# Kernel tuning notes

Hardware: AMD Instinct MI355X
Metric: run time of the kernel (lower is better)

Reference implementation:

```python
import jax, jax.numpy as jnp
import numpy as np

B, L = 2, 1024
V, D_MODEL, NL = 32, 256, 6
DI, DS, DC, DTR = 512, 16, 4, 16  # d_inner=expand*d_model, d_state, d_conv, dt_rank=d_model/16
NC, MAXL = 10, 2048
ALPHA = 0.1  # observer_alpha


def setup_inputs() -> dict:
    key = jax.random.key(0)
    ks = jax.random.split(key, 16)
    std = 0.02
    emb = std * jax.random.normal(ks[0], (V, D_MODEL), jnp.float32)
    emb = emb.at[0].set(0.0)  # padding_idx=0
    pos_emb = std * jax.random.normal(ks[1], (MAXL, D_MODEL), jnp.float32)
    ln_w = jnp.ones((NL, D_MODEL), jnp.float32)
    ln_b = jnp.zeros((NL, D_MODEL), jnp.float32)
    in_proj_w = std * jax.random.normal(ks[2], (NL, 2 * DI, D_MODEL), jnp.float32)
    conv_w = 0.1 * jax.random.normal(ks[3], (NL, DI, DC), jnp.float32)
    conv_b = jnp.zeros((NL, DI), jnp.float32)
    x_proj_w = std * jax.random.normal(ks[4], (NL, DTR + 2 * DS, DI), jnp.float32)
    dt_proj_w = std * jax.random.normal(ks[5], (NL, DI, DTR), jnp.float32)
    dt_proj_b = jnp.full((NL, DI), -4.6, jnp.float32)  # softplus(-4.6) ~ 0.01 init dt
    A_log = jnp.broadcast_to(jnp.log(jnp.arange(1, DS + 1, dtype=jnp.float32)), (NL, DI, DS)).copy()  # S4D-real
    Dp = jnp.ones((NL, DI), jnp.float32)
    out_proj_w = std * jax.random.normal(ks[6], (NL, D_MODEL, DI), jnp.float32)
    norm_w = jnp.ones((D_MODEL,), jnp.float32)
    norm_b = jnp.zeros((D_MODEL,), jnp.float32)
    cls_w = std * jax.random.normal(ks[7], (NC, D_MODEL), jnp.float32)
    cls_b = jnp.zeros((NC,), jnp.float32)
    x = jax.random.randint(ks[8], (B, L), 0, V, jnp.int64 if jax.config.jax_enable_x64 else jnp.int32)
    mask = jnp.ones((B, L), jnp.int32)
    return dict(emb=emb, pos_emb=pos_emb, ln_w=ln_w, ln_b=ln_b, in_proj_w=in_proj_w,
                conv_w=conv_w, conv_b=conv_b, x_proj_w=x_proj_w, dt_proj_w=dt_proj_w,
                dt_proj_b=dt_proj_b, A_log=A_log, Dp=Dp, out_proj_w=out_proj_w,
                norm_w=norm_w, norm_b=norm_b, cls_w=cls_w, cls_b=cls_b, x=x, mask=mask)


def _ln(x, w, b):
    m = x.mean(-1, keepdims=True)
    v = ((x - m) ** 2).mean(-1, keepdims=True)
    return (x - m) / jnp.sqrt(v + 1e-5) * w + b


def _forward(emb, pos_emb, ln_w, ln_b, in_proj_w, conv_w, conv_b, x_proj_w,
             dt_proj_w, dt_proj_b, A_log, Dp, out_proj_w, norm_w, norm_b,
             cls_w, cls_b, x, mask):
    Bsz, Lsz = x.shape
    h = emb[x] + pos_emb[:Lsz][None, :, :]  # [B,L,D]
    for i in range(NL):
        res = h
        hn = _ln(h, ln_w[i], ln_b[i])
        xz = hn @ in_proj_w[i].T                      # [B,L,2*DI]
        x_in, z = jnp.split(xz, 2, axis=-1)
        # causal depthwise conv1d, kernel DC
        xpad = jnp.pad(x_in, ((0, 0), (DC - 1, 0), (0, 0)))
        xc = conv_b[i]
        for k in range(DC):
            xc = xc + conv_w[i][:, k] * xpad[:, k:k + Lsz, :]
        xc = jax.nn.silu(xc)
        x_dbl = xc @ x_proj_w[i].T                    # [B,L,DTR+2*DS]
        dt = x_dbl[..., :DTR]
        Bm = x_dbl[..., DTR:DTR + DS]
        Cm = x_dbl[..., DTR + DS:]
        delta = jax.nn.softplus(dt @ dt_proj_w[i].T + dt_proj_b[i])  # [B,L,DI]
        A = -jnp.exp(A_log[i])                        # [DI,DS]
        dA = jnp.exp(delta[..., None] * A)            # [B,L,DI,DS]
        dBu = delta[..., None] * Bm[:, :, None, :] * xc[..., None]

        def step(carry, inp):
            hs, hh = carry
            dA_t, dBu_t, c_t = inp
            hs = dA_t * hs + dBu_t                    # true state
            pred = dA_t * hh + dBu_t                  # observer prediction
            hh = pred + ALPHA * (hs - pred)           # Luenberger correction
            y = jnp.einsum('bdn,bn->bd', hh, c_t)
            return (hs, hh), y

        init = (jnp.zeros((Bsz, DI, DS), xc.dtype), jnp.zeros((Bsz, DI, DS), xc.dtype))
        _, ys = jax.lax.scan(step, init,
                             (jnp.moveaxis(dA, 1, 0), jnp.moveaxis(dBu, 1, 0), jnp.moveaxis(Cm, 1, 0)))
        y = jnp.moveaxis(ys, 0, 1) + Dp[i] * xc       # [B,L,DI]
        y = y * jax.nn.silu(z)
        h = y @ out_proj_w[i].T + res
    mf = mask[..., None].astype(h.dtype)
    pooled = (h * mf).sum(axis=1) / mf.sum(axis=1)    # masked mean pool
    pooled = _ln(pooled, norm_w, norm_b)
    return pooled @ cls_w.T + cls_b                   # [B,NC]


def reference(emb, pos_emb, ln_w, ln_b, in_proj_w, conv_w, conv_b, x_proj_w,
              dt_proj_w, dt_proj_b, A_log, Dp, out_proj_w, norm_w, norm_b,
              cls_w, cls_b, x, mask):
    return _forward(emb, pos_emb, ln_w, ln_b, in_proj_w, conv_w, conv_b, x_proj_w,
                    dt_proj_w, dt_proj_b, A_log, Dp, out_proj_w, norm_w, norm_b,
                    cls_w, cls_b, x, mask)
```

## Files before the change

### kernel.cpp

```cpp
#include <hip/hip_runtime.h>
#include <math.h>

#define B_ 2
#define L_ 1024
#define DM 256
#define NL_ 6
#define DI_ 512
#define DS_ 16
#define DC_ 4
#define NC_ 10
#define ALPHA_ 0.1f
#define LC 32
#define NCH (L_/LC)
#define NCHAIN (B_*DI_*DS_)
#define BETA_LC 0.034336838202925124f

typedef unsigned short ushort_t;
typedef __attribute__((ext_vector_type(8))) short s16x8;
typedef __attribute__((ext_vector_type(4))) float f32x4;
typedef __attribute__((ext_vector_type(8))) unsigned short u16x8;

__device__ __forceinline__ float sigmoidf_(float x){ return 1.f/(1.f+__expf(-x)); }
__device__ __forceinline__ ushort_t f2bf(float f){
  union{float f;unsigned u;} c; c.f=f; unsigned u=c.u;
  return (ushort_t)((u + 0x7fffu + ((u>>16)&1u))>>16);
}
__device__ __forceinline__ float bf2f(ushort_t h){
  union{unsigned u;float f;} c; c.u = ((unsigned)h)<<16; return c.f;
}

__global__ void k_embed(const float* __restrict__ emb, const float* __restrict__ pos,
                        const int* __restrict__ ids, float* __restrict__ h){
  int row = blockIdx.x;
  int t = row & (L_-1);
  int d = threadIdx.x;
  int v = ids[row];
  h[(size_t)row*DM + d] = emb[(size_t)v*DM + d] + pos[(size_t)t*DM + d];
}

__global__ void k_cvt(const float* __restrict__ in, ushort_t* __restrict__ o, int n){
  int i = (blockIdx.x*256 + threadIdx.x)*4;
  if (i < n){
    float4 v = *reinterpret_cast<const float4*>(&in[i]);
    ushort4 r;
    r.x = f2bf(v.x); r.y = f2bf(v.y); r.z = f2bf(v.z); r.w = f2bf(v.w);
    *reinterpret_cast<ushort4*>(&o[i]) = r;
  }
}

__global__ __launch_bounds__(256) void k_gemm_ln(const float* __restrict__ h,
    const ushort_t* __restrict__ W, const float* __restrict__ lw,
    const float* __restrict__ lb, ushort_t* __restrict__ xzb){
  __shared__ ushort_t As[64][264];
  __shared__ ushort_t Ws[64][264];
  int bm = blockIdx.y<<6, bn = blockIdx.x<<6;
  int tid = threadIdx.x;
  {
    int r = tid>>2, q = tid&3;
    const float* src = &h[(size_t)(bm+r)*DM + q*64];
    float4 v[16]; float s1=0.f, s2=0.f;
    #pragma unroll
    for (int i=0;i<16;i++){
      v[i] = *reinterpret_cast<const float4*>(src + i*4);
      s1 += v[i].x+v[i].y+v[i].z+v[i].w;
      s2 += v[i].x*v[i].x+v[i].y*v[i].y+v[i].z*v[i].z+v[i].w*v[i].w;
    }
    s1 += __shfl_xor(s1,1); s2 += __shfl_xor(s2,1);
    s1 += __shfl_xor(s1,2); s2 += __shfl_xor(s2,2);
    float mean = s1*(1.f/DM);
    float rstd = rsqrtf(s2*(1.f/DM) - mean*mean + 1e-5f);
    #pragma unroll
    for (int i=0;i<16;i++){
      int c = q*64 + i*4;
      ushort4 o;
      o.x = f2bf((v[i].x-mean)*rstd*lw[c+0]+lb[c+0]);
      o.y = f2bf((v[i].y-mean)*rstd*lw[c+1]+lb[c+1]);
      o.z = f2bf((v[i].z-mean)*rstd*lw[c+2]+lb[c+2]);
      o.w = f2bf((v[i].w-mean)*rstd*lw[c+3]+lb[c+3]);
      *reinterpret_cast<ushort4*>(&As[r][c]) = o;
    }
    const ushort_t* ws = &W[(size_t)(bn+r)*DM + q*64];
    #pragma unroll
    for (int i=0;i<8;i++)
      *reinterpret_cast<u16x8*>(&Ws[r][q*64+i*8]) = *reinterpret_cast<const u16x8*>(ws + i*8);
  }
  __syncthreads();
  int lane = tid&63, wid = tid>>6;
  int wm = (wid>>1)<<5, wn = (wid&1)<<5;
  int fr = lane&15, fk = (lane>>4)<<3;
  f32x4 acc[2][2] = {};
  #pragma unroll
  for (int k0=0;k0<DM;k0+=32){
    s16x8 a0 = *reinterpret_cast<const s16x8*>(&As[wm+fr][k0+fk]);
    s16x8 a1 = *reinterpret_cast<const s16x8*>(&As[wm+16+fr][k0+fk]);
    s16x8 b0 = *reinterpret_cast<const s16x8*>(&Ws[wn+fr][k0+fk]);
    s16x8 b1 = *reinterpret_cast<const s16x8*>(&Ws[wn+16+fr][k0+fk]);
    acc[0][0] = __builtin_amdgcn_mfma_f32_16x16x32_bf16(a0,b0,acc[0][0],0,0,0);
    acc[0][1] = __builtin_amdgcn_mfma_f32_16x16x32_bf16(a0,b1,acc[0][1],0,0,0);
    acc[1][0] = __builtin_amdgcn_mfma_f32_16x16x32_bf16(a1,b0,acc[1][0],0,0,0);
    acc[1][1] = __builtin_amdgcn_mfma_f32_16x16x32_bf16(a1,b1,acc[1][1],0,0,0);
  }
  int cr = (lane>>4)<<2, cc = lane&15;
  #pragma unroll
  for (int i=0;i<2;i++)
    #pragma unroll
    for (int j=0;j<2;j++){
      int row = bm + wm + (i<<4) + cr;
      int col = bn + wn + (j<<4) + cc;
      #pragma unroll
      for (int r=0;r<4;r++)
        xzb[(size_t)(row+r)*(2*DI_) + col] = f2bf(acc[i][j][r]);
    }
}

__global__ __launch_bounds__(256) void k_xpc(const ushort_t* __restrict__ xzb,
    const float* __restrict__ cw, const float* __restrict__ cb,
    const float* __restrict__ xw, const float* __restrict__ dtw,
    const float* __restrict__ dtb, float* __restrict__ xc,
    float* __restrict__ xdbl, float* __restrict__ delta){
  __shared__ float sxz[7][DI_];
  __shared__ float sx[4][DI_];
  __shared__ float sdbl[4][48];
  int tid = threadIdx.x;
  int m0 = blockIdx.x*4;
  #pragma unroll
  for (int idx=0; idx<14; ++idx){
    int flat = idx*256 + tid;
    int i = flat>>9, d = flat&511;
    int mr = m0 - 3 + i;
    sxz[i][d] = (mr>=0) ? bf2f(xzb[(size_t)mr*(2*DI_) + d]) : 0.f;
  }
  __syncthreads();
  #pragma unroll
  for (int idx=0; idx<8; ++idx){
    int flat = idx*256 + tid;
    int r = flat>>9, d = flat&511;
    int t = (m0 + r) & (L_-1);
    float acc = cb[d];
    #pragma unroll
    for (int k=0;k<4;k++)
      if (t-3+k >= 0) acc = fmaf(cw[d*4+k], sxz[r+k][d], acc);
    float sv = acc * sigmoidf_(acc);
    sx[r][d] = sv;
    xc[(size_t)(m0+r)*DI_ + d] = sv;
  }
  __syncthreads();
  if (tid < 192){
    int o = tid>>2, q = tid&3;
    const float* wp = &xw[(size_t)o*DI_ + q*128];
    float a0=0.f,a1=0.f,a2=0.f,a3=0.f;
    #pragma unroll 8
    for (int k4=0;k4<32;k4++){
      float4 wv = *reinterpret_cast<const float4*>(wp + k4*4);
      int kk = q*128 + k4*4;
      float4 x0 = *reinterpret_cast<const float4*>(&sx[0][kk]);
      float4 x1 = *reinterpret_cast<const float4*>(&sx[1][kk]);
      float4 x2 = *reinterpret_cast<const float4*>(&sx[2][kk]);
      float4 x3 = *reinterpret_cast<const float4*>(&sx[3][kk]);
      a0 = fmaf(x0.x,wv.x,a0); a0 = fmaf(x0.y,wv.y,a0); a0 = fmaf(x0.z,wv.z,a0); a0 = fmaf(x0.w,wv.w,a0);
      a1 = fmaf(x1.x,wv.x,a1); a1 = fmaf(x1.y,wv.y,a1); a1 = fmaf(x1.z,wv.z,a1); a1 = fmaf(x1.w,wv.w,a1);
      a2 = fmaf(x2.x,wv.x,a2); a2 = fmaf(x2.y,wv.y,a2); a2 = fmaf(x2.z,wv.z,a2); a2 = fmaf(x2.w,wv.w,a2);
      a3 = fmaf(x3.x,wv.x,a3); a3 = fmaf(x3.y,wv.y,a3); a3 = fmaf(x3.z,wv.z,a3); a3 = fmaf(x3.w,wv.w,a3);
    }
    a0 += __shfl_xor(a0,1); a0 += __shfl_xor(a0,2);
    a1 += __shfl_xor(a1,1); a1 += __shfl_xor(a1,2);
    a2 += __shfl_xor(a2,1); a2 += __shfl_xor(a2,2);
    a3 += __shfl_xor(a3,1); a3 += __shfl_xor(a3,2);
    if (q==0){
      sdbl[0][o]=a0; sdbl[1][o]=a1; sdbl[2][o]=a2; sdbl[3][o]=a3;
      xdbl[(size_t)(m0+0)*48+o]=a0;
      xdbl[(size_t)(m0+1)*48+o]=a1;
      xdbl[(size_t)(m0+2)*48+o]=a2;
      xdbl[(size_t)(m0+3)*48+o]=a3;
    }
  }
  __syncthreads();
  #pragma unroll
  for (int idx=0; idx<8; ++idx){
    int flat = idx*256 + tid;
    int r = flat>>9, n = flat&511;
    const float4* wp = reinterpret_cast<const float4*>(&dtw[n*16]);
    float4 w0=wp[0], w1=wp[1], w2=wp[2], w3=wp[3];
    const float* sd = sdbl[r];
    float acc = dtb[n];
    acc = fmaf(sd[0],w0.x,acc);  acc = fmaf(sd[1],w0.y,acc);
    acc = fmaf(sd[2],w0.z,acc);  acc = fmaf(sd[3],w0.w,acc);
    acc = fmaf(sd[4],w1.x,acc);  acc = fmaf(sd[5],w1.y,acc);
    acc = fmaf(sd[6],w1.z,acc);  acc = fmaf(sd[7],w1.w,acc);
    acc = fmaf(sd[8],w2.x,acc);  acc = fmaf(sd[9],w2.y,acc);
    acc = fmaf(sd[10],w2.z,acc); acc = fmaf(sd[11],w2.w,acc);
    acc = fmaf(sd[12],w3.x,acc); acc = fmaf(sd[13],w3.y,acc);
    acc = fmaf(sd[14],w3.z,acc); acc = fmaf(sd[15],w3.w,acc);
    delta[(size_t)(m0+r)*DI_ + n] = (acc>20.f)? acc : log1pf(__expf(acc));
  }
}

__global__ __launch_bounds__(256) void k_scanA(const float* __restrict__ delta,
    const float* __restrict__ xc, const float* __restrict__ xdbl,
    const float* __restrict__ A_log, float* __restrict__ cpArr,
    float* __restrict__ slocArr, float* __restrict__ hlocArr){
  int j = blockIdx.x, g = blockIdx.y, b = blockIdx.z;
  int tid = threadIdx.x;
  int n = tid&15, dg = tid>>4;
  int d0 = g*16;
  __shared__ float sdel[LC][16], sxv[LC][16], sB[LC][16];
  #pragma unroll
  for (int idx=0; idx<2; ++idx){
    int flat = idx*256 + tid;
    int t = flat>>4, c = flat&15;
    int m = b*L_ + j*LC + t;
    sdel[t][c] = delta[(size_t)m*DI_ + d0 + c];
    sxv[t][c]  = xc  [(size_t)m*DI_ + d0 + c];
    sB[t][c]   = xdbl[(size_t)m*48 + 16 + c];
  }
  __syncthreads();
  float a = -__expf(A_log[(d0+dg)*DS_ + n]);
  float dA[LC], dBu[LC];
  #pragma unroll
  for (int t=0;t<LC;t++){
    float dv = sdel[t][dg];
    dA[t]  = __expf(dv*a);
    dBu[t] = dv * sxv[t][dg] * sB[t][n];
  }
  float hs=0.f, hh=0.f, cp=1.f;
  #pragma unroll
  for (int t=0;t<LC;t++){
    float mix = fmaf(ALPHA_, hs-hh, hh);
    hs = fmaf(dA[t], hs, dBu[t]);
    hh = fmaf(dA[t], mix, dBu[t]);
    cp *= dA[t];
  }
  size_t o = (size_t)j*NCHAIN + (size_t)(b*DI_+d0)*DS_ + tid;
  cpArr[o]=cp; slocArr[o]=hs; hlocArr[o]=hh;
}

__global__ __launch_bounds__(256) void k_scanC(const float* __restrict__ delta,
    const float* __restrict__ xc, const float* __restrict__ xdbl,
    const ushort_t* __restrict__ xzb, const float* __restrict__ A_log,
    const float* __restrict__ Dp, const float* __restrict__ cpArr,
    const float* __restrict__ slocArr, const float* __restrict__ hlocArr,
    ushort_t* __restrict__ y2b){
  int j = blockIdx.x, g = blockIdx.y, b = blockIdx.z;
  int tid = threadIdx.x;
  int n = tid&15, dg = tid>>4;
  int d0 = g*16;
  __shared__ float sdel[LC][16], sxv[LC][16], sB[LC][16], sC[LC][16], sz[LC][16], sy[LC][16];
  #pragma unroll
  for (int idx=0; idx<2; ++idx){
    int flat = idx*256 + tid;
    int t = flat>>4, c = flat&15;
    int m = b*L_ + j*LC + t;
    sdel[t][c] = delta[(size_t)m*DI_ + d0 + c];
    sxv[t][c]  = xc  [(size_t)m*DI_ + d0 + c];
    sB[t][c]   = xdbl[(size_t)m*48 + 16 + c];
    sC[t][c]   = xdbl[(size_t)m*48 + 32 + c];
    sz[t][c]   = bf2f(xzb[(size_t)m*(2*DI_) + DI_ + d0 + c]);
  }
  int chain = (b*DI_+d0)*DS_ + tid;
  float hs=0.f, hh=0.f;
  #pragma unroll 4
  for (int jj=0; jj<j; ++jj){
    size_t o = (size_t)jj*NCHAIN + chain;
    float cp = cpArr[o], sl = slocArr[o], hl = hlocArr[o];
    float snew = fmaf(cp, hs, sl);
    hh = fmaf(cp, fmaf(BETA_LC, hh-hs, hs), hl);
    hs = snew;
  }
  __syncthreads();
  float a = -__expf(A_log[(d0+dg)*DS_ + n]);
  float dA[LC], dBu[LC];
  #pragma unroll
  for (int t=0;t<LC;t++){
    float dv = sdel[t][dg];
    dA[t]  = __expf(dv*a);
    dBu[t] = dv * sxv[t][dg] * sB[t][n];
  }
  float yv[LC];
  #pragma unroll
  for (int t=0;t<LC;t++){
    float mix = fmaf(ALPHA_, hs-hh, hh);
    hs = fmaf(dA[t], hs, dBu[t]);
    hh = fmaf(dA[t], mix, dBu[t]);
    yv[t] = hh * sC[t][n];
  }
  #pragma unroll
  for (int t=0;t<LC;t++){
    yv[t] += __shfl_xor(yv[t],1,16);
    yv[t] += __shfl_xor(yv[t],2,16);
    yv[t] += __shfl_xor(yv[t],4,16);
    yv[t] += __shfl_xor(yv[t],8,16);
  }
  if (n==0){
    #pragma unroll
    for (int t=0;t<LC;t++) sy[t][dg] = yv[t];
  }
  __syncthreads();
  float dpv = Dp[d0 + (tid&15)];
  #pragma unroll
  for (int idx=0; idx<2; ++idx){
    int flat = idx*256 + tid;
    int t2 = flat>>4, dd = flat&15;
    float xvv = sxv[t2][dd];
    float zv  = sz [t2][dd];
    float yfin = (sy[t2][dd] + dpv*xvv) * (zv*sigmoidf_(zv));
    y2b[(size_t)(b*L_ + j*LC + t2)*DI_ + d0 + dd] = f2bf(yfin);
  }
}

__global__ __launch_bounds__(256) void k_gemm_out(const ushort_t* __restrict__ A,
    const ushort_t* __restrict__ W, float* __restrict__ h){
  __shared__ ushort_t As[32][264];
  __shared__ ushort_t Ws[64][264];
  int bm = blockIdx.y<<5, bn = blockIdx.x<<6;
  int tid = threadIdx.x;
  int lane = tid&63, wid = tid>>6;
  int wm = (wid>>1)<<4, wn = (wid&1)<<5;
  int fr = lane&15, fk = (lane>>4)<<3;
  f32x4 acc[2] = {};
  for (int k0=0;k0<DI_;k0+=256){
    {
      int r = tid>>3, q = tid&7;
      const ushort_t* src = &A[(size_t)(bm+r)*DI_ + k0 + q*32];
      #pragma unroll
      for (int i=0;i<4;i++)
        *reinterpret_cast<u16x8*>(&As[r][q*32+i*8]) = *reinterpret_cast<const u16x8*>(src+i*8);
      int r2 = tid>>2, q2 = tid&3;
      const ushort_t* ws = &W[(size_t)(bn+r2)*DI_ + k0 + q2*64];
      #pragma unroll
      for (int i=0;i<8;i++)
        *reinterpret_cast<u16x8*>(&Ws[r2][q2*64+i*8]) = *reinterpret_cast<const u16x8*>(ws+i*8);
    }
    __syncthreads();
    #pragma unroll
    for (int k=0;k<256;k+=32){
      s16x8 a0 = *reinterpret_cast<const s16x8*>(&As[wm+fr][k+fk]);
      s16x8 b0 = *reinterpret_cast<const s16x8*>(&Ws[wn+fr][k+fk]);
      s16x8 b1 = *reinterpret_cast<const s16x8*>(&Ws[wn+16+fr][k+fk]);
      acc[0] = __builtin_amdgcn_mfma_f32_16x16x32_bf16(a0,b0,acc[0],0,0,0);
      acc[1] = __builtin_amdgcn_mfma_f32_16x16x32_bf16(a0,b1,acc[1],0,0,0);
    }
    __syncthreads();
  }
  int cr = (lane>>4)<<2, cc = lane&15;
  #pragma unroll
  for (int jj=0;jj<2;jj++){
    int row = bm + wm + cr;
    int col = bn + wn + (jj<<4) + cc;
    #pragma unroll
    for (int r=0;r<4;r++){
      size_t idx2 = (size_t)(row+r)*DM + col;
      h[idx2] += acc[jj][r];
    }
  }
}

__global__ __launch_bounds__(256) void k_pool(const float* __restrict__ h,
    const int* __restrict__ mask, float* __restrict__ partial){
  int p = blockIdx.x, b = blockIdx.y, d = threadIdx.x;
  int t0 = p*64;
  __shared__ float sm[64];
  if (d < 64) sm[d] = (float)mask[b*L_ + t0 + d];
  __syncthreads();
  const float* hp = &h[(size_t)(b*L_ + t0)*DM + d];
  float s = 0.f;
  #pragma unroll 8
  for (int i=0;i<64;i++)
    s = fmaf(sm[i], hp[(size_t)i*DM], s);
  partial[(size_t)(b*16+p)*DM + d] = s;
}

__global__ __launch_bounds__(256) void k_head(const float* __restrict__ partial,
    const int* __restrict__ mask, const float* __restrict__ nw, const float* __restrict__ nb,
    const float* __restrict__ cw, const float* __restrict__ cb, float* __restrict__ out){
  int b = blockIdx.x, d = threadIdx.x;
  int4 mi = *reinterpret_cast<const int4*>(&mask[b*L_ + d*4]);
  float cnt = (float)(mi.x + mi.y + mi.z + mi.w);
  #pragma unroll
  for (int o=32;o>0;o>>=1) cnt += __shfl_down(cnt,o);
  __shared__ float ac[4];
  __shared__ float scnt;
  int wid = d>>6, lane = d&63;
  if (lane==0) ac[wid] = cnt;
  __syncthreads();
  if (d==0) scnt = ac[0]+ac[1]+ac[2]+ac[3];
  __syncthreads();
  float s = 0.f;
  #pragma unroll
  for (int p=0;p<16;p++) s += partial[(size_t)(b*16+p)*DM + d];
  float v = s / scnt;
  float s1 = v, s2 = v*v;
  #pragma unroll
  for (int o=32;o>0;o>>=1){ s1 += __shfl_down(s1,o); s2 += __shfl_down(s2,o); }
  __shared__ float a1[4], a2[4];
  __shared__ float mv[2];
  if (lane==0){ a1[wid]=s1; a2[wid]=s2; }
  __syncthreads();
  if (d==0){
    float t1=a1[0]+a1[1]+a1[2]+a1[3];
    float t2=a2[0]+a2[1]+a2[2]+a2[3];
    float m = t1/(float)DM;
    mv[0]=m; mv[1]=rsqrtf(t2/(float)DM - m*m + 1e-5f);
  }
  __syncthreads();
  __shared__ float sp[DM];
  sp[d] = (v-mv[0])*mv[1]*nw[d]+nb[d];
  __syncthreads();
  __shared__ float cpart[NC_][16];
  if (d < NC_*16){
    int c = d>>4, q = d&15;
    float acc = 0.f;
    #pragma unroll
    for (int k=0;k<16;k++) acc = fmaf(sp[q*16+k], cw[(size_t)c*DM+q*16+k], acc);
    cpart[c][q] = acc;
  }
  __syncthreads();
  if (d < NC_){
    float acc = cb[d];
    #pragma unroll
    for (int q=0;q<16;q++) acc += cpart[d][q];
    out[b*NC_+d] = acc;
  }
}

extern "C" void kernel_launch(void* const* d_in, const int* in_sizes, int n_in,
                              void* d_out, int out_size, void* d_ws, size_t ws_size,
                              hipStream_t stream){
  const float* emb   = (const float*)d_in[0];
  const float* pos   = (const float*)d_in[1];
  const float* ln_w  = (const float*)d_in[2];
  const float* ln_b  = (const float*)d_in[3];
  const float* ipw   = (const float*)d_in[4];
  const float* cw    = (const float*)d_in[5];
  const float* cb    = (const float*)d_in[6];
  const float* xpw   = (const float*)d_in[7];
  const float* dtw   = (const float*)d_in[8];
  const float* dtb   = (const float*)d_in[9];
  const float* A_log = (const float*)d_in[10];
  const float* Dp    = (const float*)d_in[11];
  const float* opw   = (const float*)d_in[12];
  const float* nw    = (const float*)d_in[13];
  const float* nb    = (const float*)d_in[14];
  const float* clw   = (const float*)d_in[15];
  const float* clb   = (const float*)d_in[16];
  const int*   ids   = (const int*)d_in[17];
  const int*   mask  = (const int*)d_in[18];
  float* out = (float*)d_out;

  float* ws    = (float*)d_ws;
  float* h     = ws;
  float* xc    = h + 524288;
  float* xdbl  = xc + 1048576;
  float* delta = xdbl + 98304;
  float* cpA   = delta + 1048576;
  float* slocA = cpA + 524288;
  float* hlocA = slocA + 524288;
  float* part  = hlocA + 524288;
  ushort_t* xzb  = (ushort_t*)(part + 8192);
  ushort_t* y2b  = xzb + 2097152;
  ushort_t* ipwb = y2b + 1048576;
  ushort_t* opwb = ipwb + 1572864;

  k_cvt<<<dim3(1536), 256, 0, stream>>>(ipw, ipwb, 6*2*DI_*DM);
  k_cvt<<<dim3(768),  256, 0, stream>>>(opw, opwb, 6*DM*DI_);
  k_embed<<<dim3(B_*L_), dim3(DM), 0, stream>>>(emb, pos, ids, h);

  for (int l=0; l<NL_; ++l){
    k_gemm_ln<<<dim3(16, 32), 256, 0, stream>>>(
        h, ipwb + (size_t)l*2*DI_*DM, ln_w + l*DM, ln_b + l*DM, xzb);
    k_xpc<<<dim3((B_*L_)/4), 256, 0, stream>>>(
        xzb, cw + l*DI_*DC_, cb + l*DI_, xpw + (size_t)l*48*DI_,
        dtw + (size_t)l*DI_*16, dtb + l*DI_, xc, xdbl, delta);
    k_scanA<<<dim3(NCH, DI_/16, B_), 256, 0, stream>>>(
        delta, xc, xdbl, A_log + (size_t)l*DI_*DS_, cpA, slocA, hlocA);
    k_scanC<<<dim3(NCH, DI_/16, B_), 256, 0, stream>>>(
        delta, xc, xdbl, xzb, A_log + (size_t)l*DI_*DS_, Dp + l*DI_,
        cpA, slocA, hlocA, y2b);
    k_gemm_out<<<dim3(DM/64, (B_*L_)/32), 256, 0, stream>>>(
        y2b, opwb + (size_t)l*DM*DI_, h);
  }
  k_pool<<<dim3(16, B_), 256, 0, stream>>>(h, mask, part);
  k_head<<<dim3(B_), 256, 0, stream>>>(part, mask, nw, nb, clw, clb, out);
}
```

Baseline: 479.1 us.

## Store scan inputs in bf16, pack chunk summaries, vectorize loads, merge weight conversion

xc and delta are now stored as bf16 instead of fp32, and scanA/scanC load them with 16-byte vector reads. The per-chunk summaries (cp, hs, hh) are packed into one float4 array instead of three separate arrays. The scan loops run in 8-step slabs to lower register pressure, the x-proj shared array is padded to avoid bank conflicts, and the two weight-conversion launches are merged into one. The intent is to cut global memory traffic and launch overhead, at the cost of bf16 rounding of delta and xc before the scan, which adds numerical error.

```diff
diff --git a/kernel.cpp b/kernel.cpp
--- a/kernel.cpp
+++ b/kernel.cpp
@@ -28,6 +28,7 @@
 __device__ __forceinline__ float bf2f(ushort_t h){
   union{unsigned u;float f;} c; c.u = ((unsigned)h)<<16; return c.f;
 }
+__device__ __forceinline__ int kidx(int d){ return d + ((d>>7)<<2); }
 
 __global__ void k_embed(const float* __restrict__ emb, const float* __restrict__ pos,
                         const int* __restrict__ ids, float* __restrict__ h){
@@ -38,14 +39,17 @@
   h[(size_t)row*DM + d] = emb[(size_t)v*DM + d] + pos[(size_t)t*DM + d];
 }
 
-__global__ void k_cvt(const float* __restrict__ in, ushort_t* __restrict__ o, int n){
+__global__ void k_cvt2(const float* __restrict__ a, int na, const float* __restrict__ b2,
+                       ushort_t* __restrict__ oa, ushort_t* __restrict__ ob, int ntot){
   int i = (blockIdx.x*256 + threadIdx.x)*4;
-  if (i < n){
-    float4 v = *reinterpret_cast<const float4*>(&in[i]);
-    ushort4 r;
-    r.x = f2bf(v.x); r.y = f2bf(v.y); r.z = f2bf(v.z); r.w = f2bf(v.w);
-    *reinterpret_cast<ushort4*>(&o[i]) = r;
-  }
+  if (i >= ntot) return;
+  const float* src; ushort_t* dst; int k;
+  if (i < na){ src = a; dst = oa; k = i; }
+  else       { src = b2; dst = ob; k = i - na; }
+  float4 v = *reinterpret_cast<const float4*>(&src[k]);
+  ushort4 r;
+  r.x = f2bf(v.x); r.y = f2bf(v.y); r.z = f2bf(v.z); r.w = f2bf(v.w);
+  *reinterpret_cast<ushort4*>(&dst[k]) = r;
 }
 
 __global__ __launch_bounds__(256) void k_gemm_ln(const float* __restrict__ h,
@@ -116,10 +120,10 @@
 __global__ __launch_bounds__(256) void k_xpc(const ushort_t* __restrict__ xzb,
     const float* __restrict__ cw, const float* __restrict__ cb,
     const float* __restrict__ xw, const float* __restrict__ dtw,
-    const float* __restrict__ dtb, float* __restrict__ xc,
-    float* __restrict__ xdbl, float* __restrict__ delta){
+    const float* __restrict__ dtb, ushort_t* __restrict__ xcb,
+    float* __restrict__ xdbl, ushort_t* __restrict__ deltab){
   __shared__ float sxz[7][DI_];
-  __shared__ float sx[4][DI_];
+  __shared__ float sx[4][DI_+16];
   __shared__ float sdbl[4][48];
   int tid = threadIdx.x;
   int m0 = blockIdx.x*4;
@@ -141,18 +145,19 @@
     for (int k=0;k<4;k++)
       if (t-3+k >= 0) acc = fmaf(cw[d*4+k], sxz[r+k][d], acc);
     float sv = acc * sigmoidf_(acc);
-    sx[r][d] = sv;
-    xc[(size_t)(m0+r)*DI_ + d] = sv;
+    sx[r][kidx(d)] = sv;
+    xcb[(size_t)(m0+r)*DI_ + d] = f2bf(sv);
   }
   __syncthreads();
   if (tid < 192){
     int o = tid>>2, q = tid&3;
     const float* wp = &xw[(size_t)o*DI_ + q*128];
+    const int qb = q*132;
     float a0=0.f,a1=0.f,a2=0.f,a3=0.f;
     #pragma unroll 8
     for (int k4=0;k4<32;k4++){
       float4 wv = *reinterpret_cast<const float4*>(wp + k4*4);
-      int kk = q*128 + k4*4;
+      int kk = qb + k4*4;
       float4 x0 = *reinterpret_cast<const float4*>(&sx[0][kk]);
       float4 x1 = *reinterpret_cast<const float4*>(&sx[1][kk]);
       float4 x2 = *reinterpret_cast<const float4*>(&sx[2][kk]);
@@ -191,108 +196,132 @@
     acc = fmaf(sd[10],w2.z,acc); acc = fmaf(sd[11],w2.w,acc);
     acc = fmaf(sd[12],w3.x,acc); acc = fmaf(sd[13],w3.y,acc);
     acc = fmaf(sd[14],w3.z,acc); acc = fmaf(sd[15],w3.w,acc);
-    delta[(size_t)(m0+r)*DI_ + n] = (acc>20.f)? acc : log1pf(__expf(acc));
-  }
-}
-
-__global__ __launch_bounds__(256) void k_scanA(const float* __restrict__ delta,
-    const float* __restrict__ xc, const float* __restrict__ xdbl,
-    const float* __restrict__ A_log, float* __restrict__ cpArr,
-    float* __restrict__ slocArr, float* __restrict__ hlocArr){
+    float sp2 = (acc>20.f)? acc : log1pf(__expf(acc));
+    deltab[(size_t)(m0+r)*DI_ + n] = f2bf(sp2);
+  }
+}
+
+__global__ __launch_bounds__(256) void k_scanA(const ushort_t* __restrict__ deltab,
+    const ushort_t* __restrict__ xcb, const float* __restrict__ xdbl,
+    const float* __restrict__ A_log, float4* __restrict__ smry){
   int j = blockIdx.x, g = blockIdx.y, b = blockIdx.z;
   int tid = threadIdx.x;
   int n = tid&15, dg = tid>>4;
   int d0 = g*16;
   __shared__ float sdel[LC][16], sxv[LC][16], sB[LC][16];
-  #pragma unroll
-  for (int idx=0; idx<2; ++idx){
-    int flat = idx*256 + tid;
-    int t = flat>>4, c = flat&15;
-    int m = b*L_ + j*LC + t;
-    sdel[t][c] = delta[(size_t)m*DI_ + d0 + c];
-    sxv[t][c]  = xc  [(size_t)m*DI_ + d0 + c];
-    sB[t][c]   = xdbl[(size_t)m*48 + 16 + c];
+  if (tid < 128){
+    int arr = tid>>6, slot = tid&63, row = slot>>1, half = slot&1;
+    int m = b*L_ + j*LC + row;
+    const ushort_t* src = arr ? xcb : deltab;
+    u16x8 v = *reinterpret_cast<const u16x8*>(&src[(size_t)m*DI_ + d0 + half*8]);
+    float* dst = arr ? &sxv[row][half*8] : &sdel[row][half*8];
+    #pragma unroll
+    for (int i=0;i<8;i++) dst[i] = bf2f((ushort_t)v[i]);
+  } else {
+    int slot = tid-128;
+    int row = slot>>2, c4 = (slot&3)<<2;
+    int m = b*L_ + j*LC + row;
+    *reinterpret_cast<float4*>(&sB[row][c4]) =
+      *reinterpret_cast<const float4*>(&xdbl[(size_t)m*48 + 16 + c4]);
   }
   __syncthreads();
   float a = -__expf(A_log[(d0+dg)*DS_ + n]);
-  float dA[LC], dBu[LC];
-  #pragma unroll
-  for (int t=0;t<LC;t++){
-    float dv = sdel[t][dg];
-    dA[t]  = __expf(dv*a);
-    dBu[t] = dv * sxv[t][dg] * sB[t][n];
-  }
   float hs=0.f, hh=0.f, cp=1.f;
   #pragma unroll
-  for (int t=0;t<LC;t++){
-    float mix = fmaf(ALPHA_, hs-hh, hh);
-    hs = fmaf(dA[t], hs, dBu[t]);
-    hh = fmaf(dA[t], mix, dBu[t]);
-    cp *= dA[t];
-  }
-  size_t o = (size_t)j*NCHAIN + (size_t)(b*DI_+d0)*DS_ + tid;
-  cpArr[o]=cp; slocArr[o]=hs; hlocArr[o]=hh;
-}
-
-__global__ __launch_bounds__(256) void k_scanC(const float* __restrict__ delta,
-    const float* __restrict__ xc, const float* __restrict__ xdbl,
+  for (int tt=0; tt<LC; tt+=8){
+    float dA8[8], dBu8[8];
+    #pragma unroll
+    for (int t=0;t<8;t++){
+      float dv = sdel[tt+t][dg];
+      dA8[t]  = __expf(dv*a);
+      dBu8[t] = dv * sxv[tt+t][dg] * sB[tt+t][n];
+    }
+    #pragma unroll
+    for (int t=0;t<8;t++){
+      float mix = fmaf(ALPHA_, hs-hh, hh);
+      hs = fmaf(dA8[t], hs, dBu8[t]);
+      hh = fmaf(dA8[t], mix, dBu8[t]);
+      cp *= dA8[t];
+    }
+  }
+  smry[(size_t)j*NCHAIN + (size_t)(b*DI_+d0)*DS_ + tid] = float4{cp,hs,hh,0.f};
+}
+
+__global__ __launch_bounds__(256) void k_scanC(const ushort_t* __restrict__ deltab,
+    const ushort_t* __restrict__ xcb, const float* __restrict__ xdbl,
     const ushort_t* __restrict__ xzb, const float* __restrict__ A_log,
-    const float* __restrict__ Dp, const float* __restrict__ cpArr,
-    const float* __restrict__ slocArr, const float* __restrict__ hlocArr,
+    const float* __restrict__ Dp, const float4* __restrict__ smry,
     ushort_t* __restrict__ y2b){
   int j = blockIdx.x, g = blockIdx.y, b = blockIdx.z;
   int tid = threadIdx.x;
   int n = tid&15, dg = tid>>4;
   int d0 = g*16;
   __shared__ float sdel[LC][16], sxv[LC][16], sB[LC][16], sC[LC][16], sz[LC][16], sy[LC][16];
-  #pragma unroll
-  for (int idx=0; idx<2; ++idx){
-    int flat = idx*256 + tid;
-    int t = flat>>4, c = flat&15;
-    int m = b*L_ + j*LC + t;
-    sdel[t][c] = delta[(size_t)m*DI_ + d0 + c];
-    sxv[t][c]  = xc  [(size_t)m*DI_ + d0 + c];
-    sB[t][c]   = xdbl[(size_t)m*48 + 16 + c];
-    sC[t][c]   = xdbl[(size_t)m*48 + 32 + c];
-    sz[t][c]   = bf2f(xzb[(size_t)m*(2*DI_) + DI_ + d0 + c]);
+  if (tid < 128){
+    int arr = tid>>6, slot = tid&63, row = slot>>1, half = slot&1;
+    int m = b*L_ + j*LC + row;
+    const ushort_t* src = arr ? xcb : deltab;
+    u16x8 v = *reinterpret_cast<const u16x8*>(&src[(size_t)m*DI_ + d0 + half*8]);
+    float* dst = arr ? &sxv[row][half*8] : &sdel[row][half*8];
+    #pragma unroll
+    for (int i=0;i<8;i++) dst[i] = bf2f((ushort_t)v[i]);
+  } else if (tid < 192){
+    int slot = tid-128, row = slot>>1, half = slot&1;
+    int m = b*L_ + j*LC + row;
+    u16x8 v = *reinterpret_cast<const u16x8*>(&xzb[(size_t)m*(2*DI_) + DI_ + d0 + half*8]);
+    #pragma unroll
+    for (int i=0;i<8;i++) sz[row][half*8+i] = bf2f((ushort_t)v[i]);
+  } else {
+    int slot = tid-192;
+    #pragma unroll
+    for (int k=0;k<4;k++){
+      int t4 = slot + k*64;
+      int arr = t4>>7, idx4 = t4&127;
+      int row = idx4>>2, c4 = (idx4&3)<<2;
+      int m = b*L_ + j*LC + row;
+      float* dst = arr ? &sC[row][c4] : &sB[row][c4];
+      *reinterpret_cast<float4*>(dst) =
+        *reinterpret_cast<const float4*>(&xdbl[(size_t)m*48 + 16 + arr*16 + c4]);
+    }
   }
   int chain = (b*DI_+d0)*DS_ + tid;
   float hs=0.f, hh=0.f;
   #pragma unroll 4
   for (int jj=0; jj<j; ++jj){
-    size_t o = (size_t)jj*NCHAIN + chain;
-    float cp = cpArr[o], sl = slocArr[o], hl = hlocArr[o];
-    float snew = fmaf(cp, hs, sl);
-    hh = fmaf(cp, fmaf(BETA_LC, hh-hs, hs), hl);
+    float4 v = smry[(size_t)jj*NCHAIN + chain];
+    float snew = fmaf(v.x, hs, v.y);
+    hh = fmaf(v.x, fmaf(BETA_LC, hh-hs, hs), v.z);
     hs = snew;
   }
   __syncthreads();
   float a = -__expf(A_log[(d0+dg)*DS_ + n]);
-  float dA[LC], dBu[LC];
-  #pragma unroll
-  for (int t=0;t<LC;t++){
-    float dv = sdel[t][dg];
-    dA[t]  = __expf(dv*a);
-    dBu[t] = dv * sxv[t][dg] * sB[t][n];
-  }
-  float yv[LC];
-  #pragma unroll
-  for (int t=0;t<LC;t++){
-    float mix = fmaf(ALPHA_, hs-hh, hh);
-    hs = fmaf(dA[t], hs, dBu[t]);
-    hh = fmaf(dA[t], mix, dBu[t]);
-    yv[t] = hh * sC[t][n];
-  }
-  #pragma unroll
-  for (int t=0;t<LC;t++){
-    yv[t] += __shfl_xor(yv[t],1,16);
-    yv[t] += __shfl_xor(yv[t],2,16);
-    yv[t] += __shfl_xor(yv[t],4,16);
-    yv[t] += __shfl_xor(yv[t],8,16);
-  }
-  if (n==0){
-    #pragma unroll
-    for (int t=0;t<LC;t++) sy[t][dg] = yv[t];
+  #pragma unroll
+  for (int tt=0; tt<LC; tt+=8){
+    float dA8[8], dBu8[8], yv8[8];
+    #pragma unroll
+    for (int t=0;t<8;t++){
+      float dv = sdel[tt+t][dg];
+      dA8[t]  = __expf(dv*a);
+      dBu8[t] = dv * sxv[tt+t][dg] * sB[tt+t][n];
+    }
+    #pragma unroll
+    for (int t=0;t<8;t++){
+      float mix = fmaf(ALPHA_, hs-hh, hh);
+      hs = fmaf(dA8[t], hs, dBu8[t]);
+      hh = fmaf(dA8[t], mix, dBu8[t]);
+      yv8[t] = hh * sC[tt+t][n];
+    }
+    #pragma unroll
+    for (int t=0;t<8;t++){
+      yv8[t] += __shfl_xor(yv8[t],1,16);
+      yv8[t] += __shfl_xor(yv8[t],2,16);
+      yv8[t] += __shfl_xor(yv8[t],4,16);
+      yv8[t] += __shfl_xor(yv8[t],8,16);
+    }
+    if (n==0){
+      #pragma unroll
+      for (int t=0;t<8;t++) sy[tt+t][dg] = yv8[t];
+    }
   }
   __syncthreads();
   float dpv = Dp[d0 + (tid&15)];
@@ -448,20 +477,18 @@
 
   float* ws    = (float*)d_ws;
   float* h     = ws;
-  float* xc    = h + 524288;
-  float* xdbl  = xc + 1048576;
-  float* delta = xdbl + 98304;
-  float* cpA   = delta + 1048576;
-  float* slocA = cpA + 524288;
-  float* hlocA = slocA + 524288;
-  float* part  = hlocA + 524288;
-  ushort_t* xzb  = (ushort_t*)(part + 8192);
-  ushort_t* y2b  = xzb + 2097152;
-  ushort_t* ipwb = y2b + 1048576;
-  ushort_t* opwb = ipwb + 1572864;
-
-  k_cvt<<<dim3(1536), 256, 0, stream>>>(ipw, ipwb, 6*2*DI_*DM);
-  k_cvt<<<dim3(768),  256, 0, stream>>>(opw, opwb, 6*DM*DI_);
+  float* xdbl  = h + 524288;
+  float* part  = xdbl + 98304;
+  float4* smry = (float4*)(part + 8192);
+  ushort_t* xzb    = (ushort_t*)((float*)smry + 2097152);
+  ushort_t* xcb    = xzb + 2097152;
+  ushort_t* deltab = xcb + 1048576;
+  ushort_t* y2b    = deltab + 1048576;
+  ushort_t* ipwb   = y2b + 1048576;
+  ushort_t* opwb   = ipwb + 1572864;
+
+  const int NA = 6*2*DI_*DM, NB = 6*DM*DI_;
+  k_cvt2<<<dim3((NA+NB)/1024), 256, 0, stream>>>(ipw, NA, opw, ipwb, opwb, NA+NB);
   k_embed<<<dim3(B_*L_), dim3(DM), 0, stream>>>(emb, pos, ids, h);
 
   for (int l=0; l<NL_; ++l){
@@ -469,12 +496,12 @@
         h, ipwb + (size_t)l*2*DI_*DM, ln_w + l*DM, ln_b + l*DM, xzb);
     k_xpc<<<dim3((B_*L_)/4), 256, 0, stream>>>(
         xzb, cw + l*DI_*DC_, cb + l*DI_, xpw + (size_t)l*48*DI_,
-        dtw + (size_t)l*DI_*16, dtb + l*DI_, xc, xdbl, delta);
+        dtw + (size_t)l*DI_*16, dtb + l*DI_, xcb, xdbl, deltab);
     k_scanA<<<dim3(NCH, DI_/16, B_), 256, 0, stream>>>(
-        delta, xc, xdbl, A_log + (size_t)l*DI_*DS_, cpA, slocA, hlocA);
+        deltab, xcb, xdbl, A_log + (size_t)l*DI_*DS_, smry);
     k_scanC<<<dim3(NCH, DI_/16, B_), 256, 0, stream>>>(
-        delta, xc, xdbl, xzb, A_log + (size_t)l*DI_*DS_, Dp + l*DI_,
-        cpA, slocA, hlocA, y2b);
+        deltab, xcb, xdbl, xzb, A_log + (size_t)l*DI_*DS_, Dp + l*DI_,
+        smry, y2b);
     k_gemm_out<<<dim3(DM/64, (B_*L_)/32), 256, 0, stream>>>(
         y2b, opwb + (size_t)l*DM*DI_, h);
   }
```

New measurement: 477.3 us. Within noise of the previous version (-0.4%).
